# Performance work log

Hardware: AMD Instinct MI355X
Metric: run time of the kernel (lower is better)

The kernel has to match this reference:

```python
import jax, jax.numpy as jnp
import numpy as np

NN_SIZE = 10  # k nearest neighbors (includes the point itself)
EPS = 1e-8


def batch_normals(points_nchw, nn_size):
    # points_nchw: (B, 3, N)
    x = jnp.transpose(points_nchw, (0, 2, 1))  # (B, N, 3)
    sq = jnp.sum(x * x, axis=-1)  # (B, N)
    # pairwise squared distances (B, N, N)
    d2 = sq[:, :, None] + sq[:, None, :] - 2.0 * jnp.einsum('bnd,bmd->bnm', x, x)
    _, idx = jax.lax.top_k(-d2, nn_size)  # (B, N, k) nearest-neighbor indices
    # irregular gather of neighborhoods: (B, N, k, 3)
    neigh = jax.vmap(lambda p, i: p[i])(x, idx)
    centered = neigh - jnp.mean(neigh, axis=2, keepdims=True)
    # local 3x3 covariance per point
    cov = jnp.einsum('bnki,bnkj->bnij', centered, centered) / nn_size
    _, vecs = jnp.linalg.eigh(cov)  # eigenvalues ascending
    normals = vecs[..., 0]  # eigenvector of smallest eigenvalue, (B, N, 3), unit norm
    return jnp.transpose(normals, (0, 2, 1))  # (B, 3, N)


def setup_inputs() -> dict:
    key = jax.random.key(0)
    k1, k2 = jax.random.split(key)
    pred = jax.random.normal(k1, (8, 3, 4096), dtype=jnp.float32)
    gt = jax.random.normal(k2, (8, 3, 4096), dtype=jnp.float32)
    return {"pred": pred, "gt": gt}


def reference(pred, gt):
    pn = batch_normals(pred, NN_SIZE)  # (B, 3, N)
    gn = batch_normals(gt, NN_SIZE)    # (B, 3, N)
    # cosine similarity along the channel (coordinate) dim
    dot = jnp.sum(pn * gn, axis=1)
    denom = jnp.sqrt(jnp.sum(pn * pn, axis=1)) * jnp.sqrt(jnp.sum(gn * gn, axis=1))
    cos = dot / jnp.maximum(denom, EPS)
    return jnp.mean(1.0 - jnp.abs(cos))
```

## Files before the change

kernel.cpp:

```cpp
#include <hip/hip_runtime.h>
#include <float.h>
#include <math.h>

#define BATCH 8
#define NPTS 4096
#define KNN 10
#define BN (BATCH * NPTS)
#define TPB 1024
#define WAVES 16
#define Q 2
#define QPB (64 * Q)
#define SEGC (NPTS / WAVES)
#define KB_STRIDE (Q * KNN + 1)

__device__ float4 g_nrm[2 * BN];

__device__ inline float med3f(float x, float a, float b) {
    return __builtin_amdgcn_fmed3f(x, a, b);
}

#define INSERT(karr, key)                                              \
    do {                                                               \
        _Pragma("unroll")                                              \
        for (int _j = KNN - 1; _j >= 1; --_j)                          \
            karr[_j] = med3f((key), karr[_j - 1], karr[_j]);           \
        karr[0] = fminf((key), karr[0]);                               \
    } while (0)

#define PROC(_p, _gi)                                                  \
    do {                                                               \
        float _d0 = fmaf((_p).z, a0z, fmaf((_p).y, a0y, fmaf((_p).x, a0x, (_p).w))); \
        float _d1 = fmaf((_p).z, a1z, fmaf((_p).y, a1y, fmaf((_p).x, a1x, (_p).w))); \
        float _k0 = __uint_as_float((__float_as_uint(_d0) & 0xFFFFF000u) | (_gi)); \
        float _k1 = __uint_as_float((__float_as_uint(_d1) & 0xFFFFF000u) | (_gi)); \
        INSERT(kq0, _k0);                                              \
        INSERT(kq1, _k1);                                              \
    } while (0)

#define PROC2(P, _gi)                                                  \
    do {                                                               \
        PROC(P##0, (_gi) + 0);                                         \
        PROC(P##1, (_gi) + 1);                                         \
    } while (0)

#define LOAD2(P, _off)                                                 \
    do {                                                               \
        P##0 = pts[(_off) + 0]; P##1 = pts[(_off) + 1];                \
    } while (0)

__device__ inline void smallest_eigvec(float a00, float a01, float a02,
                                       float a11, float a12, float a22,
                                       float& vx, float& vy, float& vz) {
    float p1 = a01 * a01 + a02 * a02 + a12 * a12;
    float q = (a00 + a11 + a22) * (1.0f / 3.0f);
    float b00 = a00 - q, b11 = a11 - q, b22 = a22 - q;
    float p2 = b00 * b00 + b11 * b11 + b22 * b22 + 2.0f * p1;
    float p = sqrtf(p2 * (1.0f / 6.0f));
    if (p < 1e-20f) { vx = 1.0f; vy = 0.0f; vz = 0.0f; return; }
    float ip = 1.0f / p;
    float c00 = b00 * ip, c01 = a01 * ip, c02 = a02 * ip;
    float c11 = b11 * ip, c12 = a12 * ip, c22 = b22 * ip;
    float detB = c00 * (c11 * c22 - c12 * c12)
               - c01 * (c01 * c22 - c12 * c02)
               + c02 * (c01 * c12 - c11 * c02);
    float r = 0.5f * detB;
    r = fminf(1.0f, fmaxf(-1.0f, r));
    float phi = acosf(r) * (1.0f / 3.0f);
    float lmin = q + 2.0f * p * cosf(phi + 2.0943951023931953f);

    float m00 = a00 - lmin, m11 = a11 - lmin, m22 = a22 - lmin;
    float r0x = m00, r0y = a01, r0z = a02;
    float r1x = a01, r1y = m11, r1z = a12;
    float r2x = a02, r2y = a12, r2z = m22;
    float c0x = r0y * r1z - r0z * r1y, c0y = r0z * r1x - r0x * r1z, c0z = r0x * r1y - r0y * r1x;
    float c1x = r0y * r2z - r0z * r2y, c1y = r0z * r2x - r0x * r2z, c1z = r0x * r2y - r0y * r2x;
    float c2x = r1y * r2z - r1z * r2y, c2y = r1z * r2x - r1x * r2z, c2z = r1x * r2y - r1y * r2x;
    float n0 = c0x * c0x + c0y * c0y + c0z * c0z;
    float n1 = c1x * c1x + c1y * c1y + c1z * c1z;
    float n2 = c2x * c2x + c2y * c2y + c2z * c2z;
    float bx = c0x, by = c0y, bz = c0z, bnm = n0;
    if (n1 > bnm) { bx = c1x; by = c1y; bz = c1z; bnm = n1; }
    if (n2 > bnm) { bx = c2x; by = c2y; bz = c2z; bnm = n2; }
    if (bnm < 1e-30f) { vx = 1.0f; vy = 0.0f; vz = 0.0f; return; }
    float inv = rsqrtf(bnm);
    vx = bx * inv; vy = by * inv; vz = bz * inv;
}

__global__ void zero_out_kernel(float* __restrict__ out) {
    if (threadIdx.x == 0) out[0] = 0.0f;
}

__global__ __launch_bounds__(TPB, 8) void knn_normals(
    const float* __restrict__ pred, const float* __restrict__ gt) {
    __shared__ float4 pts[NPTS + 8];
    float* keybuf = (float*)pts;

    const int b = blockIdx.y;
    const int cloud = blockIdx.z;
    const float* __restrict__ base = (cloud ? gt : pred) + b * 3 * NPTS;
    const int tid = threadIdx.x;
    const int lane = tid & 63;
    const int w = tid >> 6;
    const int s0 = w * SEGC;
    const int qbase = blockIdx.x * QPB;

    for (int i = tid; i < NPTS; i += TPB) {
        float x = base[i];
        float y = base[NPTS + i];
        float z = base[2 * NPTS + i];
        pts[i] = make_float4(x, y, z, fmaf(x, x, fmaf(y, y, z * z)));
    }
    __syncthreads();

    const int q0 = qbase + lane;
    const float a0x = -2.0f * pts[q0].x,      a0y = -2.0f * pts[q0].y,      a0z = -2.0f * pts[q0].z;
    const float a1x = -2.0f * pts[q0 + 64].x, a1y = -2.0f * pts[q0 + 64].y, a1z = -2.0f * pts[q0 + 64].z;

    float kq0[KNN], kq1[KNN];
#pragma unroll
    for (int j = 0; j < KNN; ++j) { kq0[j] = FLT_MAX; kq1[j] = FLT_MAX; }

    {
        const unsigned gb = (unsigned)s0;
        float4 A0, A1, B0, B1;
        LOAD2(A, s0);
        __builtin_amdgcn_sched_barrier(0);
        for (int c = 0; c < SEGC; c += 4) {
            LOAD2(B, s0 + c + 2);
            __builtin_amdgcn_sched_barrier(0);
            PROC2(A, gb + (unsigned)c);
            __builtin_amdgcn_sched_barrier(0);
            LOAD2(A, s0 + c + 4);
            __builtin_amdgcn_sched_barrier(0);
            PROC2(B, gb + (unsigned)c + 2u);
            __builtin_amdgcn_sched_barrier(0);
        }
    }
    __syncthreads();

    for (int half = WAVES / 2; half >= 1; half >>= 1) {
        if (w >= half && w < 2 * half) {
            float* dst = keybuf + ((w - half) * 64 + lane) * KB_STRIDE;
#pragma unroll
            for (int j = 0; j < KNN; ++j) { dst[j] = kq0[j]; dst[KNN + j] = kq1[j]; }
        }
        __syncthreads();
        if (w < half) {
            const float* src = keybuf + (w * 64 + lane) * KB_STRIDE;
#pragma unroll
            for (int j = 0; j < KNN; ++j) {
                float s0v = src[j], s1v = src[KNN + j];
                INSERT(kq0, s0v);
                INSERT(kq1, s1v);
            }
        }
        __syncthreads();
    }

    if (w == 0) {
        float* dst = keybuf + lane * KB_STRIDE;
#pragma unroll
        for (int j = 0; j < KNN; ++j) { dst[j] = kq0[j]; dst[KNN + j] = kq1[j]; }
    }
    __syncthreads();
    if (w < Q) {
        const float* src = keybuf + lane * KB_STRIDE + w * KNN;
        float sx = 0.f, sy = 0.f, sz = 0.f;
        float sxx = 0.f, sxy = 0.f, sxz = 0.f;
        float syy = 0.f, syz = 0.f, szz = 0.f;
#pragma unroll
        for (int j = 0; j < KNN; ++j) {
            int idx = (int)(__float_as_uint(src[j]) & 0xFFFu);
            float x = base[idx];
            float y = base[NPTS + idx];
            float z = base[2 * NPTS + idx];
            sx += x; sy += y; sz += z;
            sxx = fmaf(x, x, sxx); sxy = fmaf(x, y, sxy); sxz = fmaf(x, z, sxz);
            syy = fmaf(y, y, syy); syz = fmaf(y, z, syz); szz = fmaf(z, z, szz);
        }
        const float iK = 1.0f / KNN;
        float mx = sx * iK, my = sy * iK, mz = sz * iK;
        float vx, vy, vz;
        smallest_eigvec(sxx * iK - mx * mx, sxy * iK - mx * my,
                        sxz * iK - mx * mz, syy * iK - my * my,
                        syz * iK - my * mz, szz * iK - mz * mz,
                        vx, vy, vz);
        g_nrm[(cloud * BATCH + b) * NPTS + qbase + w * 64 + lane] = make_float4(vx, vy, vz, 0.f);
    }
}

__global__ __launch_bounds__(256) void cos_loss_kernel(float* __restrict__ out) {
    const int i = blockIdx.x * 256 + threadIdx.x;
    float4 p = g_nrm[i];
    float4 g = g_nrm[BN + i];
    float dot = p.x * g.x + p.y * g.y + p.z * g.z;
    float npn = sqrtf(p.x * p.x + p.y * p.y + p.z * p.z);
    float ngn = sqrtf(g.x * g.x + g.y * g.y + g.z * g.z);
    float acc = 1.0f - fabsf(dot / fmaxf(npn * ngn, 1e-8f));
    for (int off = 32; off > 0; off >>= 1) acc += __shfl_down(acc, off);
    if ((threadIdx.x & 63) == 0) atomicAdd(out, acc * (1.0f / (float)BN));
}

extern "C" void kernel_launch(void* const* d_in, const int* in_sizes, int n_in,
                              void* d_out, int out_size, void* d_ws, size_t ws_size,
                              hipStream_t stream) {
    const float* pred = (const float*)d_in[0];
    const float* gt = (const float*)d_in[1];
    float* out = (float*)d_out;

    zero_out_kernel<<<1, 64, 0, stream>>>(out);
    dim3 grid(NPTS / QPB, BATCH, 2);
    knn_normals<<<grid, TPB, 0, stream>>>(pred, gt);
    cos_loss_kernel<<<dim3(BN / 256), 256, 0, stream>>>(out);
}
```

Baseline: 173.0 us.

## Sort clouds by x and search kNN in expanding windows with pruning

```diff
diff --git a/kernel.cpp b/kernel.cpp
--- a/kernel.cpp
+++ b/kernel.cpp
@@ -6,13 +6,12 @@
 #define NPTS 4096
 #define KNN 10
 #define BN (BATCH * NPTS)
-#define TPB 1024
-#define WAVES 16
-#define Q 2
-#define QPB (64 * Q)
-#define SEGC (NPTS / WAVES)
-#define KB_STRIDE (Q * KNN + 1)
-
+#define NCLOUD (2 * BATCH)
+#define CHUNK 64
+#define QPB 64
+
+__device__ float4 g_spts[NCLOUD * NPTS];
+__device__ int    g_perm[NCLOUD * NPTS];
 __device__ float4 g_nrm[2 * BN];
 
 __device__ inline float med3f(float x, float a, float b) {
@@ -27,25 +26,33 @@
         karr[0] = fminf((key), karr[0]);                               \
     } while (0)
 
-#define PROC(_p, _gi)                                                  \
+#define PROC1(_p, _gi)                                                 \
     do {                                                               \
-        float _d0 = fmaf((_p).z, a0z, fmaf((_p).y, a0y, fmaf((_p).x, a0x, (_p).w))); \
-        float _d1 = fmaf((_p).z, a1z, fmaf((_p).y, a1y, fmaf((_p).x, a1x, (_p).w))); \
-        float _k0 = __uint_as_float((__float_as_uint(_d0) & 0xFFFFF000u) | (_gi)); \
-        float _k1 = __uint_as_float((__float_as_uint(_d1) & 0xFFFFF000u) | (_gi)); \
-        INSERT(kq0, _k0);                                              \
-        INSERT(kq1, _k1);                                              \
+        float _d = fmaf((_p).z, a0z, fmaf((_p).y, a0y, fmaf((_p).x, a0x, (_p).w))); \
+        float _k = __uint_as_float((__float_as_uint(_d) & 0xFFFFF000u) | (unsigned)(_gi)); \
+        INSERT(kq, _k);                                                \
     } while (0)
 
-#define PROC2(P, _gi)                                                  \
+#define RETHR() (kq[KNN - 1] + qw + fmaf(fabsf(kq[KNN - 1]), 2e-3f, 1e-4f))
+
+#define DOCHUNK(_lo)                                                   \
     do {                                                               \
-        PROC(P##0, (_gi) + 0);                                         \
-        PROC(P##1, (_gi) + 1);                                         \
-    } while (0)
-
-#define LOAD2(P, _off)                                                 \
-    do {                                                               \
-        P##0 = pts[(_off) + 0]; P##1 = pts[(_off) + 1];                \
+        wbuf[w][lane] = g_spts[cb + (_lo) + lane];                     \
+        _Pragma("unroll")                                              \
+        for (int _cc = 0; _cc < CHUNK; _cc += 8) {                     \
+            float4 C0 = wbuf[w][_cc + 0], C1 = wbuf[w][_cc + 1];       \
+            float4 C2 = wbuf[w][_cc + 2], C3 = wbuf[w][_cc + 3];       \
+            float4 C4 = wbuf[w][_cc + 4], C5 = wbuf[w][_cc + 5];       \
+            float4 C6 = wbuf[w][_cc + 6], C7 = wbuf[w][_cc + 7];       \
+            PROC1(C0, (_lo) + _cc + 0);                                \
+            PROC1(C1, (_lo) + _cc + 1);                                \
+            PROC1(C2, (_lo) + _cc + 2);                                \
+            PROC1(C3, (_lo) + _cc + 3);                                \
+            PROC1(C4, (_lo) + _cc + 4);                                \
+            PROC1(C5, (_lo) + _cc + 5);                                \
+            PROC1(C6, (_lo) + _cc + 6);                                \
+            PROC1(C7, (_lo) + _cc + 7);                                \
+        }                                                              \
     } while (0)
 
 __device__ inline void smallest_eigvec(float a00, float a01, float a02,
@@ -90,93 +97,111 @@
     if (threadIdx.x == 0) out[0] = 0.0f;
 }
 
-__global__ __launch_bounds__(TPB, 8) void knn_normals(
+__global__ __launch_bounds__(1024) void sort_clouds(
     const float* __restrict__ pred, const float* __restrict__ gt) {
-    __shared__ float4 pts[NPTS + 8];
-    float* keybuf = (float*)pts;
-
-    const int b = blockIdx.y;
-    const int cloud = blockIdx.z;
-    const float* __restrict__ base = (cloud ? gt : pred) + b * 3 * NPTS;
+    __shared__ float skey[NPTS];
+    __shared__ int   sidx[NPTS];
+    const int c = blockIdx.x;
+    const float* __restrict__ base =
+        (c >= BATCH) ? (gt + (c - BATCH) * 3 * NPTS) : (pred + c * 3 * NPTS);
     const int tid = threadIdx.x;
+
+    for (int i = tid; i < NPTS; i += 1024) { skey[i] = base[i]; sidx[i] = i; }
+
+    for (int k = 2; k <= NPTS; k <<= 1) {
+        for (int j = k >> 1; j > 0; j >>= 1) {
+            __syncthreads();
+            for (int t = tid; t < NPTS / 2; t += 1024) {
+                int i = ((t / j) * 2 * j) + (t % j);
+                int p = i + j;
+                bool up = ((i & k) == 0);
+                float a = skey[i], bb = skey[p];
+                bool sw = up ? (a > bb) : (a < bb);
+                if (sw) {
+                    skey[i] = bb; skey[p] = a;
+                    int ia = sidx[i]; sidx[i] = sidx[p]; sidx[p] = ia;
+                }
+            }
+        }
+    }
+    __syncthreads();
+
+    const int cb = c * NPTS;
+    for (int i = tid; i < NPTS; i += 1024) {
+        int idx = sidx[i];
+        float x = skey[i];
+        float y = base[NPTS + idx];
+        float z = base[2 * NPTS + idx];
+        g_spts[cb + i] = make_float4(x, y, z, fmaf(x, x, fmaf(y, y, z * z)));
+        g_perm[cb + i] = idx;
+    }
+}
+
+__global__ __launch_bounds__(128) void knn_window() {
+    __shared__ float4 wbuf[2][CHUNK];
+    __shared__ float  keybuf[QPB][KNN];
+
+    const int c  = blockIdx.x;
+    const int bx = blockIdx.y;
+    const int cb = c * NPTS;
+    const int tid  = threadIdx.x;
     const int lane = tid & 63;
-    const int w = tid >> 6;
-    const int s0 = w * SEGC;
-    const int qbase = blockIdx.x * QPB;
-
-    for (int i = tid; i < NPTS; i += TPB) {
-        float x = base[i];
-        float y = base[NPTS + i];
-        float z = base[2 * NPTS + i];
-        pts[i] = make_float4(x, y, z, fmaf(x, x, fmaf(y, y, z * z)));
+    const int w    = tid >> 6;
+    const int s0 = bx * QPB;
+    const int s  = s0 + lane;
+
+    const float4 qp = g_spts[cb + s];
+    const float qx = qp.x, qw = qp.w;
+    const float a0x = -2.0f * qp.x, a0y = -2.0f * qp.y, a0z = -2.0f * qp.z;
+
+    float kq[KNN];
+#pragma unroll
+    for (int j = 0; j < KNN; ++j) kq[j] = FLT_MAX;
+
+    DOCHUNK(s0);
+    float thr = RETHR();
+
+    if (w == 0) {
+        int lo = s0;
+        while (lo > 0) {
+            float xe = wbuf[0][0].x;
+            float dx = qx - xe;
+            if (__all(dx * dx >= thr)) break;
+            lo -= CHUNK;
+            DOCHUNK(lo);
+            thr = RETHR();
+        }
+    } else {
+        int hi = s0;
+        while (hi + CHUNK < NPTS) {
+            float xe = wbuf[1][CHUNK - 1].x;
+            float dx = xe - qx;
+            if (__all(dx * dx >= thr)) break;
+            hi += CHUNK;
+            DOCHUNK(hi);
+            thr = RETHR();
+        }
+    }
+
+    if (w == 0) {
+#pragma unroll
+        for (int j = 0; j < KNN; ++j) keybuf[lane][j] = kq[j];
     }
     __syncthreads();
-
-    const int q0 = qbase + lane;
-    const float a0x = -2.0f * pts[q0].x,      a0y = -2.0f * pts[q0].y,      a0z = -2.0f * pts[q0].z;
-    const float a1x = -2.0f * pts[q0 + 64].x, a1y = -2.0f * pts[q0 + 64].y, a1z = -2.0f * pts[q0 + 64].z;
-
-    float kq0[KNN], kq1[KNN];
-#pragma unroll
-    for (int j = 0; j < KNN; ++j) { kq0[j] = FLT_MAX; kq1[j] = FLT_MAX; }
-
-    {
-        const unsigned gb = (unsigned)s0;
-        float4 A0, A1, B0, B1;
-        LOAD2(A, s0);
-        __builtin_amdgcn_sched_barrier(0);
-        for (int c = 0; c < SEGC; c += 4) {
-            LOAD2(B, s0 + c + 2);
-            __builtin_amdgcn_sched_barrier(0);
-            PROC2(A, gb + (unsigned)c);
-            __builtin_amdgcn_sched_barrier(0);
-            LOAD2(A, s0 + c + 4);
-            __builtin_amdgcn_sched_barrier(0);
-            PROC2(B, gb + (unsigned)c + 2u);
-            __builtin_amdgcn_sched_barrier(0);
-        }
-    }
-    __syncthreads();
-
-    for (int half = WAVES / 2; half >= 1; half >>= 1) {
-        if (w >= half && w < 2 * half) {
-            float* dst = keybuf + ((w - half) * 64 + lane) * KB_STRIDE;
-#pragma unroll
-            for (int j = 0; j < KNN; ++j) { dst[j] = kq0[j]; dst[KNN + j] = kq1[j]; }
-        }
-        __syncthreads();
-        if (w < half) {
-            const float* src = keybuf + (w * 64 + lane) * KB_STRIDE;
-#pragma unroll
-            for (int j = 0; j < KNN; ++j) {
-                float s0v = src[j], s1v = src[KNN + j];
-                INSERT(kq0, s0v);
-                INSERT(kq1, s1v);
-            }
-        }
-        __syncthreads();
-    }
-
-    if (w == 0) {
-        float* dst = keybuf + lane * KB_STRIDE;
-#pragma unroll
-        for (int j = 0; j < KNN; ++j) { dst[j] = kq0[j]; dst[KNN + j] = kq1[j]; }
-    }
-    __syncthreads();
-    if (w < Q) {
-        const float* src = keybuf + lane * KB_STRIDE + w * KNN;
+    if (w == 1) {
+#pragma unroll
+        for (int j = 0; j < KNN; ++j) { float v = keybuf[lane][j]; INSERT(kq, v); }
+
         float sx = 0.f, sy = 0.f, sz = 0.f;
         float sxx = 0.f, sxy = 0.f, sxz = 0.f;
         float syy = 0.f, syz = 0.f, szz = 0.f;
 #pragma unroll
         for (int j = 0; j < KNN; ++j) {
-            int idx = (int)(__float_as_uint(src[j]) & 0xFFFu);
-            float x = base[idx];
-            float y = base[NPTS + idx];
-            float z = base[2 * NPTS + idx];
-            sx += x; sy += y; sz += z;
-            sxx = fmaf(x, x, sxx); sxy = fmaf(x, y, sxy); sxz = fmaf(x, z, sxz);
-            syy = fmaf(y, y, syy); syz = fmaf(y, z, syz); szz = fmaf(z, z, szz);
+            int sidx = (int)(__float_as_uint(kq[j]) & 0xFFFu);
+            float4 nb = g_spts[cb + sidx];
+            sx += nb.x; sy += nb.y; sz += nb.z;
+            sxx = fmaf(nb.x, nb.x, sxx); sxy = fmaf(nb.x, nb.y, sxy); sxz = fmaf(nb.x, nb.z, sxz);
+            syy = fmaf(nb.y, nb.y, syy); syz = fmaf(nb.y, nb.z, syz); szz = fmaf(nb.z, nb.z, szz);
         }
         const float iK = 1.0f / KNN;
         float mx = sx * iK, my = sy * iK, mz = sz * iK;
@@ -185,7 +210,9 @@
                         sxz * iK - mx * mz, syy * iK - my * my,
                         syz * iK - my * mz, szz * iK - mz * mz,
                         vx, vy, vz);
-        g_nrm[(cloud * BATCH + b) * NPTS + qbase + w * 64 + lane] = make_float4(vx, vy, vz, 0.f);
+        const int cs = c >> 3, b = c & 7;
+        const int oq = g_perm[cb + s];
+        g_nrm[cs * BN + b * NPTS + oq] = make_float4(vx, vy, vz, 0.f);
     }
 }
 
@@ -209,7 +236,7 @@
     float* out = (float*)d_out;
 
     zero_out_kernel<<<1, 64, 0, stream>>>(out);
-    dim3 grid(NPTS / QPB, BATCH, 2);
-    knn_normals<<<grid, TPB, 0, stream>>>(pred, gt);
+    sort_clouds<<<dim3(NCLOUD), 1024, 0, stream>>>(pred, gt);
+    knn_window<<<dim3(NCLOUD, NPTS / QPB), 128, 0, stream>>>();
     cos_loss_kernel<<<dim3(BN / 256), 256, 0, stream>>>(out);
 }
```

Measured after the change: 266.9 us. +54.3%, slower.
